# Optimization experiments

Hardware: AMD Instinct MI355X
Metric: run time of the kernel (lower is better)

Reference implementation:

```python
import jax, jax.numpy as jnp
import numpy as np

DIM = 192
HEADS = 8
B, H, W = 2, 256, 256
CPH = DIM // HEADS  # 24 channels per head
EPS = 1e-12

_SOB_DX = np.array([[1, 0, 1], [-2, 0, 2], [-1, 0, 1]], np.float32)
_SOB_DY = np.array([[1, -2, -1], [0, 0, 0], [1, 2, 1]], np.float32)


def _conv2d(x, w, pad, groups=1):
    return jax.lax.conv_general_dilated(
        x, w, window_strides=(1, 1), padding=[(pad, pad), (pad, pad)],
        dimension_numbers=('NCHW', 'OIHW', 'NCHW'), feature_group_count=groups)


def _l2norm(t):
    n = jnp.sqrt(jnp.sum(t * t, axis=-1, keepdims=True))
    return t / jnp.maximum(n, EPS)


def _topk_masked_softmax(attn, k):
    # attn: [B, HEADS, C, C]; keep top-k entries per row, softmax over them.
    b, h, c, _ = attn.shape
    idx = jax.lax.top_k(attn, k)[1]                      # [B,H,C,k]
    flat_idx = idx.reshape(-1, k)
    rows = jnp.arange(flat_idx.shape[0])[:, None]
    mask = jnp.zeros((b * h * c, c), bool).at[rows, flat_idx].set(True)
    masked = jnp.where(mask.reshape(attn.shape), attn, -jnp.inf)
    return jax.nn.softmax(masked, axis=-1)


def setup_inputs() -> dict:
    key = jax.random.key(0)
    ks = jax.random.split(key, 6)
    s = 0.02
    return {
        'x': jax.random.normal(ks[0], (B, DIM, H, W), jnp.float32),
        'q_w': jax.random.normal(ks[1], (DIM, DIM, 1, 1), jnp.float32) * s,
        'q_dw': jax.random.normal(ks[2], (DIM, 1, 3, 3), jnp.float32) * s,
        'kv_w': jax.random.normal(ks[3], (2 * DIM, DIM, 1, 1), jnp.float32) * s,
        'kv_dw': jax.random.normal(ks[4], (2 * DIM, 1, 3, 3), jnp.float32) * s,
        'proj_w': jax.random.normal(ks[5], (DIM, DIM, 1, 1), jnp.float32) * s,
        'temperature': jnp.ones((HEADS, 1, 1), jnp.float32),
        'a1': jnp.full((1,), 0.2, jnp.float32),
        'a2': jnp.full((1,), 0.2, jnp.float32),
        'a3': jnp.full((1,), 0.2, jnp.float32),
        'a4': jnp.full((1,), 0.2, jnp.float32),
    }


def reference(x, q_w, q_dw, kv_w, kv_dw, proj_w, temperature, a1, a2, a3, a4):
    b, c, h, w = x.shape
    # Sob: dense (dim,dim,3,3) Sobel convs (kernel broadcast over all in-channels)
    dx_w = jnp.broadcast_to(jnp.asarray(_SOB_DX), (c, c, 3, 3))
    dy_w = jnp.broadcast_to(jnp.asarray(_SOB_DY), (c, c, 3, 3))
    dx = _conv2d(x, dx_w, 1)
    dy = _conv2d(x, dy_w, 1)

    q_s = _conv2d(_conv2d(dx + dy, q_w, 0), q_dw, 1, groups=c)
    kv = _conv2d(_conv2d(x, kv_w, 0), kv_dw, 1, groups=2 * c)
    k_, v = kv[:, :c], kv[:, c:]

    hw = h * w
    q_s = _l2norm(q_s.reshape(b, HEADS, CPH, hw))
    k_ = _l2norm(k_.reshape(b, HEADS, CPH, hw))
    v = v.reshape(b, HEADS, CPH, hw)

    # channel attention: [B, HEADS, C, C]
    attn = jnp.einsum('bhcn,bhdn->bhcd', q_s, k_) * temperature

    C = CPH
    out = (a1 * (_topk_masked_softmax(attn, int(C / 2)) @ v)
           + a2 * (_topk_masked_softmax(attn, int(C * 2 / 3)) @ v)
           + a3 * (_topk_masked_softmax(attn, int(C * 3 / 4)) @ v)
           + a4 * (_topk_masked_softmax(attn, int(C * 4 / 5)) @ v))

    out = out.reshape(b, c, h, w)
    return _conv2d(out, proj_w, 0)
```

## Files before the change

kernel.cpp:

```cpp
#include <hip/hip_runtime.h>
#include <math.h>

#define NH 8
#define HWv 65536
#define C2 384

typedef __attribute__((ext_vector_type(8))) short bf16x8;
typedef __attribute__((ext_vector_type(4))) float f32x4;

__device__ __forceinline__ float bf2f(unsigned short u) {
    union { unsigned int i; float f; } v; v.i = ((unsigned int)u) << 16; return v.f;
}
__device__ __forceinline__ unsigned short f2bf(float f) {
    union { float f; unsigned int i; } v; v.f = f;
    unsigned int r = v.i + 0x7fff + ((v.i >> 16) & 1);
    return (unsigned short)(r >> 16);
}
__device__ __forceinline__ float hi_of(float a) {
    union { float f; unsigned int i; } u; u.f = a; u.i &= 0xffff0000u; return u.f;
}
__device__ __forceinline__ unsigned short hi16(float a) {
    union { float f; unsigned int i; } u; u.f = a; return (unsigned short)(u.i >> 16);
}
__device__ __forceinline__ unsigned int pack_hi2(float a, float b) {
    union { float f; unsigned int i; } ua, ub; ua.f = a; ub.f = b;
    return (ua.i >> 16) | (ub.i & 0xffff0000u);
}
__device__ __forceinline__ void gld16(const void* g, void* l) {
    __builtin_amdgcn_global_load_lds(
        (const __attribute__((address_space(1))) unsigned int*)g,
        (__attribute__((address_space(3))) unsigned int*)l, 16, 0, 0);
}
__device__ __forceinline__ int rot4(int lb, int row) {
    return (lb + row + (row >> 2)) & 3;
}

__global__ __launch_bounds__(256) void k_wprep(const float* __restrict__ w,
                                               const float* __restrict__ qw,
                                               unsigned short* __restrict__ oh,
                                               unsigned short* __restrict__ ol,
                                               float* __restrict__ qs) {
    if (blockIdx.x == 288) {
        const int o = threadIdx.x;
        if (o < 192) {
            float s = 0.f;
            for (int i = 0; i < 192; ++i) s += qw[(size_t)o * 192 + i];
            qs[o] = s;
        }
        return;
    }
    const int i = blockIdx.x * 256 + threadIdx.x;
    const int e = i & 7, jp = (i >> 3) & 3, rowidx = i >> 5;
    const int o = rowidx % 384, ks = rowidx / 384;
    const int lb = (jp - o - (o >> 2)) & 3;
    const int k = ks * 32 + (lb << 3) + e;
    const float v = w[(size_t)o * 192 + k];
    const unsigned short h = f2bf(v);
    oh[i] = h;
    ol[i] = f2bf(v - bf2f(h));
}

__global__ __launch_bounds__(256, 2) void k_gemm(const float* __restrict__ x,
                                                 const unsigned short* __restrict__ wh,
                                                 const unsigned short* __restrict__ wl,
                                                 unsigned short* __restrict__ t,
                                                 float* __restrict__ s) {
    const int l = blockIdx.x;
    const int xcd = l & 7, idx = l >> 3;
    const int pxtile = xcd * 64 + (idx >> 1);
    const int half = idx & 1;
    const int b = blockIdx.z;
    const int p0 = pxtile * 128;
    const int woff = half * 192;
    const int tid = threadIdx.x;
    const int lane = tid & 63, wv = tid >> 6;
    const int wm2 = wv & 1, wn2 = wv >> 1;
    __shared__ __align__(16) char SU[40960];
    unsigned short* Xh  = (unsigned short*)SU;
    unsigned short* Xl  = Xh + 128 * 32;
    unsigned short* Whs = Xl + 128 * 32;
    unsigned short* Wls = Whs + 192 * 32;
    unsigned short* Ts  = (unsigned short*)SU;
    float* Ls = (float*)(SU + 26624);
    f32x4 acc[4][6];
#pragma unroll
    for (int m = 0; m < 4; ++m)
#pragma unroll
        for (int n = 0; n < 6; ++n) acc[m][n] = (f32x4){0.f, 0.f, 0.f, 0.f};
    const int px = tid & 127, cg = tid >> 7;
    const float* xb = x + (size_t)b * 192 * HWv + p0 + px;
    const int r = lane & 15, g = lane >> 4;
    const int pbx0 = rot4(2 * cg, px);
    const int pbx1 = rot4(2 * cg + 1, px);
    float csum = 0.f;
    for (int ks = 0; ks < 6; ++ks) {
        const int k0 = ks * 32;
        __syncthreads();
        {
            const char* gh  = (const char*)wh + ((size_t)(ks * 384 + woff)) * 64;
            const char* gl2 = (const char*)wl + ((size_t)(ks * 384 + woff)) * 64;
            char* lh = (char*)Whs;
            char* ll = (char*)Wls;
#pragma unroll
            for (int i = 0; i < 3; ++i) {
                const int chunk = (i * 4 + wv) * 1024;
                gld16(gh + chunk + lane * 16, lh + chunk);
                gld16(gl2 + chunk + lane * 16, ll + chunk);
            }
        }
        {
            unsigned int ph[8], pl[8];
#pragma unroll
            for (int i2 = 0; i2 < 8; ++i2) {
                const int c0 = k0 + cg * 16 + i2 * 2;
                const float v0 = xb[(size_t)c0 * HWv];
                const float v1 = xb[(size_t)(c0 + 1) * HWv];
                csum += v0 + v1;
                ph[i2] = pack_hi2(v0, v1);
                pl[i2] = pack_hi2(v0 - hi_of(v0), v1 - hi_of(v1));
            }
            *(uint4*)&Xh[px * 32 + pbx0 * 8] = make_uint4(ph[0], ph[1], ph[2], ph[3]);
            *(uint4*)&Xh[px * 32 + pbx1 * 8] = make_uint4(ph[4], ph[5], ph[6], ph[7]);
            *(uint4*)&Xl[px * 32 + pbx0 * 8] = make_uint4(pl[0], pl[1], pl[2], pl[3]);
            *(uint4*)&Xl[px * 32 + pbx1 * 8] = make_uint4(pl[4], pl[5], pl[6], pl[7]);
        }
        __syncthreads();
        bf16x8 ah[4], al[4];
#pragma unroll
        for (int m = 0; m < 4; ++m) {
            const int row = wm2 * 64 + m * 16 + r;
            const int ro = rot4(g, row) * 8;
            ah[m] = *(const bf16x8*)&Xh[row * 32 + ro];
            al[m] = *(const bf16x8*)&Xl[row * 32 + ro];
        }
#pragma unroll
        for (int n = 0; n < 6; ++n) {
            const int row = wn2 * 96 + n * 16 + r;
            const int ro = rot4(g, row) * 8;
            const bf16x8 bh = *(const bf16x8*)&Whs[row * 32 + ro];
            const bf16x8 bl = *(const bf16x8*)&Wls[row * 32 + ro];
#pragma unroll
            for (int m = 0; m < 4; ++m) {
                acc[m][n] = __builtin_amdgcn_mfma_f32_16x16x32_bf16(ah[m], bh, acc[m][n], 0, 0, 0);
                acc[m][n] = __builtin_amdgcn_mfma_f32_16x16x32_bf16(ah[m], bl, acc[m][n], 0, 0, 0);
                acc[m][n] = __builtin_amdgcn_mfma_f32_16x16x32_bf16(al[m], bh, acc[m][n], 0, 0, 0);
            }
        }
    }
    __syncthreads();
    if (half == 0) Ls[cg * 128 + px] = csum;
    __syncthreads();
    if (half == 0 && tid < 128)
        s[((size_t)b << 16) + p0 + tid] = Ls[tid] + Ls[128 + tid];
    unsigned short* tb = t + (size_t)b * HWv * C2;
#pragma unroll
    for (int ph2 = 0; ph2 < 2; ++ph2) {
        __syncthreads();
        if (wm2 == ph2) {
#pragma unroll
            for (int m = 0; m < 4; ++m)
#pragma unroll
                for (int n = 0; n < 6; ++n)
#pragma unroll
                    for (int rr = 0; rr < 4; ++rr)
                        Ts[(m * 16 + g * 4 + rr) * 200 + wn2 * 96 + n * 16 + r] =
                            f2bf(acc[m][n][rr]);
        }
        __syncthreads();
        for (int i = tid; i < 1536; i += 256) {
            const int pxl = i / 24, cho = (i % 24) * 8;
            unsigned short* dst = tb + (size_t)(p0 + ph2 * 64 + pxl) * C2 + woff + cho;
            *(uint4*)dst = *(const uint4*)&Ts[pxl * 200 + cho];
        }
    }
}

__global__ __launch_bounds__(256) void k_attn(const unsigned short* __restrict__ t,
                                              const float* __restrict__ sbuf,
                                              const float* __restrict__ qsum,
                                              const float* __restrict__ qdw,
                                              const float* __restrict__ kvdw,
                                              float* __restrict__ part) {
    const int z = blockIdx.z, b = z >> 3, h = z & 7;
    const int tid = threadIdx.x;
    const int lane = tid & 63, wv = tid >> 6;
    __shared__ __align__(16) char U[50688];
    float* ehalo = (float*)U;
    float* Thalo = (float*)(U + 1296);
    float* shalo = (float*)(U + 32496);
    unsigned short* QKh = (unsigned short*)U;
    unsigned short* QKl = QKh + 48 * 264;
    float* Pp = (float*)U;
    __shared__ float qdwl[216], kdwl[216], qsml[24];
    for (int i = tid; i < 456; i += 256) {
        if (i < 216) qdwl[i] = qdw[h * 216 + i];
        else if (i < 432) kdwl[i - 216] = kvdw[h * 216 + (i - 216)];
        else qsml[i - 432] = qsum[h * 24 + (i - 432)];
    }
    f32x4 acc[6];
#pragma unroll
    for (int tl = 0; tl < 6; ++tl) acc[tl] = (f32x4){0.f, 0.f, 0.f, 0.f};
    const int lr = tid >> 4, lc = tid & 15;
    const int r = lane & 15, g = lane >> 4;
    for (int st = 0; st < 4; ++st) {
        const int tx0 = (blockIdx.x * 2 + (st & 1)) * 16;
        const int ty0 = (blockIdx.y * 2 + (st >> 1)) * 16;
        __syncthreads();
        for (int i = tid; i < 400; i += 256) {
            const int rr = i / 20, cc = i % 20;
            const int y = ty0 - 2 + rr, xx = tx0 - 2 + cc;
            shalo[i] = (y >= 0 && y < 256 && xx >= 0 && xx < 256)
                           ? sbuf[((size_t)b << 16) + y * 256 + xx] : 0.f;
        }
        for (int i = tid; i < 972; i += 256) {
            const int p = i / 3, seg = i % 3;
            const int rr = p / 18, cc = p % 18;
            const int y = ty0 - 1 + rr, xx = tx0 - 1 + cc;
            if (y >= 0 && y < 256 && xx >= 0 && xx < 256) {
                const unsigned short* src =
                    t + ((size_t)b * HWv + y * 256 + xx) * C2 + h * 24 + seg * 8;
                const uint4 v = *(const uint4*)src;
                Thalo[(seg * 8 + 0) * 325 + p] = bf2f((unsigned short)(v.x & 0xffff));
                Thalo[(seg * 8 + 1) * 325 + p] = bf2f((unsigned short)(v.x >> 16));
                Thalo[(seg * 8 + 2) * 325 + p] = bf2f((unsigned short)(v.y & 0xffff));
                Thalo[(seg * 8 + 3) * 325 + p] = bf2f((unsigned short)(v.y >> 16));
                Thalo[(seg * 8 + 4) * 325 + p] = bf2f((unsigned short)(v.z & 0xffff));
                Thalo[(seg * 8 + 5) * 325 + p] = bf2f((unsigned short)(v.z >> 16));
                Thalo[(seg * 8 + 6) * 325 + p] = bf2f((unsigned short)(v.w & 0xffff));
                Thalo[(seg * 8 + 7) * 325 + p] = bf2f((unsigned short)(v.w >> 16));
            } else {
#pragma unroll
                for (int j = 0; j < 8; ++j) Thalo[(seg * 8 + j) * 325 + p] = 0.f;
            }
        }
        __syncthreads();
        for (int i = tid; i < 324; i += 256) {
            const int rr = i / 18, cc = i % 18;
            const int y = ty0 - 1 + rr, xx = tx0 - 1 + cc;
            const float v = (((((shalo[rr * 20 + cc]
                              - shalo[rr * 20 + cc + 1])
                              - shalo[(rr + 1) * 20 + cc])
                              + shalo[(rr + 1) * 20 + cc + 2])
                              + shalo[(rr + 2) * 20 + cc + 1])
                              + shalo[(rr + 2) * 20 + cc + 2]);
            ehalo[i] = (y >= 0 && y < 256 && xx >= 0 && xx < 256) ? 2.f * v : 0.f;
        }
        __syncthreads();
        float qreg[24], kreg[24];
#pragma unroll
        for (int c = 0; c < 24; ++c) {
            float aq = 0.f, ak = 0.f;
#pragma unroll
            for (int dy = 0; dy < 3; ++dy)
#pragma unroll
                for (int dx = 0; dx < 3; ++dx) {
                    aq = fmaf(qdwl[c * 9 + dy * 3 + dx], ehalo[(lr + dy) * 18 + lc + dx], aq);
                    ak = fmaf(kdwl[c * 9 + dy * 3 + dx], Thalo[c * 325 + (lr + dy) * 18 + lc + dx], ak);
                }
            qreg[c] = qsml[c] * aq;
            kreg[c] = ak;
        }
        __syncthreads();
#pragma unroll
        for (int c = 0; c < 24; ++c) {
            const float q = qreg[c], kv = kreg[c];
            QKh[c * 264 + tid] = hi16(q);
            QKl[c * 264 + tid] = hi16(q - hi_of(q));
            QKh[(24 + c) * 264 + tid] = hi16(kv);
            QKl[(24 + c) * 264 + tid] = hi16(kv - hi_of(kv));
        }
        __syncthreads();
#pragma unroll
        for (int c2 = 0; c2 < 2; ++c2) {
            const int colb = (wv * 2 + c2) * 32 + g * 8;
            bf16x8 fh[3], fl[3];
#pragma unroll
            for (int rt = 0; rt < 3; ++rt) {
                fh[rt] = *(const bf16x8*)&QKh[(rt * 16 + r) * 264 + colb];
                fl[rt] = *(const bf16x8*)&QKl[(rt * 16 + r) * 264 + colb];
            }
#define GRAM(T, A, B) \
    acc[T] = __builtin_amdgcn_mfma_f32_16x16x32_bf16(fh[A], fh[B], acc[T], 0, 0, 0); \
    acc[T] = __builtin_amdgcn_mfma_f32_16x16x32_bf16(fh[A], fl[B], acc[T], 0, 0, 0); \
    acc[T] = __builtin_amdgcn_mfma_f32_16x16x32_bf16(fl[A], fh[B], acc[T], 0, 0, 0);
            GRAM(0, 0, 0) GRAM(1, 0, 1) GRAM(2, 0, 2)
            GRAM(3, 1, 1) GRAM(4, 1, 2) GRAM(5, 2, 2)
#undef GRAM
        }
    }
    __syncthreads();
#pragma unroll
    for (int tl = 0; tl < 6; ++tl)
#pragma unroll
        for (int reg = 0; reg < 4; ++reg)
            Pp[wv * 1536 + tl * 256 + (g * 4 + reg) * 16 + r] = acc[tl][reg];
    __syncthreads();
    float* dst = part + ((size_t)z * 64 + blockIdx.y * 8 + blockIdx.x) * 1536;
    for (int i = tid; i < 1536; i += 256)
        dst[i] = Pp[i] + Pp[1536 + i] + Pp[3072 + i] + Pp[4608 + i];
}

__device__ __forceinline__ int gidx(int i, int j) {
    const int rt = i >> 4, ct = j >> 4;
    const int tl = (rt == 0) ? ct : (rt == 1 ? 2 + ct : 5);
    return tl * 256 + (i & 15) * 16 + (j & 15);
}

__global__ __launch_bounds__(256) void k_redcomb(const float* __restrict__ part,
                                                 const float* __restrict__ temp,
                                                 const float* __restrict__ a1,
                                                 const float* __restrict__ a2,
                                                 const float* __restrict__ a3,
                                                 const float* __restrict__ a4,
                                                 float* __restrict__ Wg) {
    const int z = blockIdx.x, b = z >> 3, h = z & 7;
    const int tid = threadIdx.x;
    __shared__ float S[1536];
    __shared__ float att[24][24];
    __shared__ float nq[24], nk[24];
    for (int i = tid; i < 1536; i += 256) {
        float sum = 0.f;
        const float* p = part + (size_t)z * 64 * 1536 + i;
        for (int blk = 0; blk < 64; ++blk) sum += p[(size_t)blk * 1536];
        S[i] = sum;
    }
    __syncthreads();
    if (tid < 24) nq[tid] = fmaxf(sqrtf(S[gidx(tid, tid)]), 1e-12f);
    else if (tid >= 32 && tid < 56) {
        const int d = tid - 32;
        nk[d] = fmaxf(sqrtf(S[gidx(24 + d, 24 + d)]), 1e-12f);
    }
    __syncthreads();
    const float tp = temp[h];
    for (int op = tid; op < 576; op += 256) {
        const int c = op / 24, d = op % 24;
        att[c][d] = S[gidx(c, 24 + d)] * tp / (nq[c] * nk[d]);
    }
    __syncthreads();
    if (tid < 24) {
        const int c = tid;
        float v[24];
#pragma unroll
        for (int d = 0; d < 24; ++d) v[d] = att[c][d];
        int rank[24];
#pragma unroll
        for (int d = 0; d < 24; ++d) {
            int rr = 0;
#pragma unroll
            for (int d2 = 0; d2 < 24; ++d2)
                rr += (v[d2] > v[d]) || (v[d2] == v[d] && d2 < d);
            rank[d] = rr;
        }
        const int ks[4] = {12, 16, 18, 19};
        const float as[4] = {a1[0], a2[0], a3[0], a4[0]};
        float w[24] = {};
        for (int ti = 0; ti < 4; ++ti) {
            const int kk = ks[ti];
            float m = -1e30f;
            for (int d = 0; d < 24; ++d) if (rank[d] < kk) m = fmaxf(m, v[d]);
            float Z = 0.f, ex[24];
            for (int d = 0; d < 24; ++d) {
                ex[d] = (rank[d] < kk) ? expf(v[d] - m) : 0.f;
                Z += ex[d];
            }
            const float sc = as[ti] / Z;
            for (int d = 0; d < 24; ++d) w[d] += ex[d] * sc;
        }
        for (int d = 0; d < 24; ++d)
            Wg[(((size_t)b * NH + h) * 24 + c) * 24 + d] = w[d];
    }
}

__global__ void k_makeM(const float* __restrict__ projw, const float* __restrict__ Wg,
                        unsigned short* __restrict__ Mh, unsigned short* __restrict__ Ml) {
    const int b = blockIdx.x / 192, o = blockIdx.x % 192;
    const int j = threadIdx.x;
    const int h = j / 24, d = j % 24;
    float s = 0.f;
#pragma unroll
    for (int cc = 0; cc < 24; ++cc)
        s = fmaf(projw[(size_t)o * 192 + h * 24 + cc],
                 Wg[(((size_t)b * NH + h) * 24 + cc) * 24 + d], s);
    const unsigned short hh = f2bf(s);
    const int jg = j >> 5, jb = (j >> 3) & 3, e = j & 7;
    const int jp = rot4(jb, o);
    const size_t dst = (((size_t)b * 6 + jg) * 192 + o) * 32 + jp * 8 + e;
    Mh[dst] = hh;
    Ml[dst] = f2bf(s - bf2f(hh));
}

__global__ __launch_bounds__(256) void k_final(const unsigned short* __restrict__ t,
                                               const float* __restrict__ kvdw,
                                               const unsigned short* __restrict__ Mh,
                                               const unsigned short* __restrict__ Ml,
                                               float* __restrict__ out) {
    const int b = blockIdx.y;
    const int tile = blockIdx.x;
    const int x0 = (tile & 15) * 16, y0 = (tile >> 4) * 4;
    const int tid = threadIdx.x;
    const int lane = tid & 63, wv = tid >> 6;
    __shared__ __align__(16) unsigned short Th[108][40];
    __shared__ __align__(16) unsigned short Msh[192 * 32], Msl[192 * 32];
    __shared__ __align__(16) unsigned short Vsh[64][40], Vsl[64][40];
    __shared__ float Wdl[288];
    f32x4 acc[3][4];
#pragma unroll
    for (int m = 0; m < 3; ++m)
#pragma unroll
        for (int n = 0; n < 4; ++n) acc[m][n] = (f32x4){0.f, 0.f, 0.f, 0.f};
    const int px = tid & 63, jq = tid >> 6;
    const int lx = px & 15, ly = px >> 4;
    const int r = lane & 15, g = lane >> 4;
    for (int jg = 0; jg < 6; ++jg) {
        const int j0 = jg * 32;
        __syncthreads();
        {
            const char* gh  = (const char*)Mh + (((size_t)b * 6 + jg) * 192) * 64;
            const char* gl2 = (const char*)Ml + (((size_t)b * 6 + jg) * 192) * 64;
            char* lh = (char*)Msh;
            char* ll = (char*)Msl;
#pragma unroll
            for (int i = 0; i < 3; ++i) {
                const int chunk = (i * 4 + wv) * 1024;
                gld16(gh + chunk + lane * 16, lh + chunk);
                gld16(gl2 + chunk + lane * 16, ll + chunk);
            }
        }
        if (tid < 216) {
            const int hp = tid >> 1, half = tid & 1;
            const int hy = hp / 18, hx = hp % 18;
            const int y = y0 - 1 + hy, xx = x0 - 1 + hx;
            uint4 v0 = make_uint4(0, 0, 0, 0), v1 = make_uint4(0, 0, 0, 0);
            if (y >= 0 && y < 256 && xx >= 0 && xx < 256) {
                const unsigned short* src =
                    t + ((size_t)b * HWv + y * 256 + xx) * C2 + 192 + j0 + half * 16;
                v0 = *(const uint4*)src;
                v1 = *(const uint4*)(src + 8);
            }
            *(uint4*)&Th[hp][half * 16] = v0;
            *(uint4*)&Th[hp][half * 16 + 8] = v1;
        }
        for (int i = tid; i < 288; i += 256) Wdl[i] = kvdw[1728 + jg * 288 + i];
        __syncthreads();
        {
            float vv[8] = {0.f, 0.f, 0.f, 0.f, 0.f, 0.f, 0.f, 0.f};
#pragma unroll
            for (int dy = 0; dy < 3; ++dy)
#pragma unroll
                for (int dx = 0; dx < 3; ++dx) {
                    const int hp = (ly + dy) * 18 + lx + dx;
                    const uint4 tv = *(const uint4*)&Th[hp][jq * 8];
                    float tf[8];
                    tf[0] = bf2f((unsigned short)(tv.x & 0xffff));
                    tf[1] = bf2f((unsigned short)(tv.x >> 16));
                    tf[2] = bf2f((unsigned short)(tv.y & 0xffff));
                    tf[3] = bf2f((unsigned short)(tv.y >> 16));
                    tf[4] = bf2f((unsigned short)(tv.z & 0xffff));
                    tf[5] = bf2f((unsigned short)(tv.z >> 16));
                    tf[6] = bf2f((unsigned short)(tv.w & 0xffff));
                    tf[7] = bf2f((unsigned short)(tv.w >> 16));
                    const int tap = dy * 3 + dx;
#pragma unroll
                    for (int jj = 0; jj < 8; ++jj)
                        vv[jj] = fmaf(Wdl[(jq * 8 + jj) * 9 + tap], tf[jj], vv[jj]);
                }
            unsigned int ph[4], pl[4];
#pragma unroll
            for (int i2 = 0; i2 < 4; ++i2) {
                const float a = vv[i2 * 2], c = vv[i2 * 2 + 1];
                ph[i2] = pack_hi2(a, c);
                pl[i2] = pack_hi2(a - hi_of(a), c - hi_of(c));
            }
            *(uint4*)&Vsh[px][jq * 8] = make_uint4(ph[0], ph[1], ph[2], ph[3]);
            *(uint4*)&Vsl[px][jq * 8] = make_uint4(pl[0], pl[1], pl[2], pl[3]);
        }
        __syncthreads();
        bf16x8 bh[4], bl[4];
#pragma unroll
        for (int n = 0; n < 4; ++n) {
            bh[n] = *(const bf16x8*)&Vsh[n * 16 + r][g * 8];
            bl[n] = *(const bf16x8*)&Vsl[n * 16 + r][g * 8];
        }
#pragma unroll
        for (int m = 0; m < 3; ++m) {
            const int row = wv * 48 + m * 16 + r;
            const int ro = rot4(g, row) * 8;
            const bf16x8 ah = *(const bf16x8*)&Msh[row * 32 + ro];
            const bf16x8 al = *(const bf16x8*)&Msl[row * 32 + ro];
#pragma unroll
            for (int n = 0; n < 4; ++n) {
                acc[m][n] = __builtin_amdgcn_mfma_f32_16x16x32_bf16(ah, bh[n], acc[m][n], 0, 0, 0);
                acc[m][n] = __builtin_amdgcn_mfma_f32_16x16x32_bf16(ah, bl[n], acc[m][n], 0, 0, 0);
                acc[m][n] = __builtin_amdgcn_mfma_f32_16x16x32_bf16(al, bh[n], acc[m][n], 0, 0, 0);
            }
        }
    }
#pragma unroll
    for (int m = 0; m < 3; ++m) {
        const int o = wv * 48 + m * 16 + g * 4;
#pragma unroll
        for (int n = 0; n < 4; ++n) {
            const int p = (y0 + n) * 256 + x0 + r;
#pragma unroll
            for (int rr = 0; rr < 4; ++rr)
                out[((size_t)b * 192 + o + rr) * HWv + p] = acc[m][n][rr];
        }
    }
}


extern "C" void kernel_launch(void* const* d_in, const int* in_sizes, int n_in,
                              void* d_out, int out_size, void* d_ws, size_t ws_size,
                              hipStream_t stream) {
    (void)in_sizes; (void)n_in; (void)out_size;
    const float* x     = (const float*)d_in[0];
    const float* qw    = (const float*)d_in[1];
    const float* qdw   = (const float*)d_in[2];
    const float* kvw   = (const float*)d_in[3];
    const float* kvdw  = (const float*)d_in[4];
    const float* projw = (const float*)d_in[5];
    const float* temp  = (const float*)d_in[6];
    const float* a1    = (const float*)d_in[7];
    const float* a2    = (const float*)d_in[8];
    const float* a3    = (const float*)d_in[9];
    const float* a4    = (const float*)d_in[10];
    float* out = (float*)d_out;

    const size_t T_EL = (size_t)2 * HWv * C2;
    const size_t needB = T_EL * 2
                       + (size_t)(131072 + 131072 + 192 + 1572864 + 24576 + 9216) * 4
                       + (size_t)(73728 * 4) * 2;
    if (ws_size < needB) return;
    unsigned short* t = (unsigned short*)d_ws;
    float* s    = (float*)(t + T_EL);
    float* e    = s + 131072;
    float* qsum = e + 131072;
    float* part = qsum + 192;
    float* accS = part + 1572864;
    float* Wg   = accS + 24576;
    unsigned short* wh = (unsigned short*)(Wg + 9216);
    unsigned short* wl = wh + 73728;
    unsigned short* Mh = wl + 73728;
    unsigned short* Ml = Mh + 73728;

    k_wprep<<<289, 256, 0, stream>>>(kvw, qw, wh, wl, qsum);
    k_gemm<<<dim3(1024, 1, 2), 256, 0, stream>>>(x, wh, wl, t, s);
    k_attn<<<dim3(8, 8, 16), 256, 0, stream>>>(t, s, qsum, qdw, kvdw, part);
    k_redcomb<<<16, 256, 0, stream>>>(part, temp, a1, a2, a3, a4, Wg);
    k_makeM<<<384, 192, 0, stream>>>(projw, Wg, Mh, Ml);
    k_final<<<dim3(1024, 2), 256, 0, stream>>>(t, kvdw, Mh, Ml, out);
}
```

Baseline: 256.1 us.

## Double-buffer weight tiles in LDS and prefetch x into registers in GEMM

The 1x1-conv GEMM kernel now keeps two LDS buffers for the hi/lo bf16 weight tiles and a two-slot register buffer for x. Each k-step issues the loads for step k+1 before converting and computing step k, so global latency overlaps with MFMA work instead of sitting behind a __syncthreads. The paired __syncthreads are replaced by raw s_barrier calls plus an explicit lgkmcnt wait. This raises LDS use from 40 KB to 64 KB per block and adds register pressure from the 32-float prefetch buffer, and it relies on compiler-inserted vmcnt waits to make the async LDS loads visible before they are read.

New measurement: 267.0 us. 4.3% more time.

```diff
diff --git a/kernel.cpp b/kernel.cpp
--- a/kernel.cpp
+++ b/kernel.cpp
@@ -75,11 +75,9 @@
     const int tid = threadIdx.x;
     const int lane = tid & 63, wv = tid >> 6;
     const int wm2 = wv & 1, wn2 = wv >> 1;
-    __shared__ __align__(16) char SU[40960];
+    __shared__ __align__(16) char SU[65536];
     unsigned short* Xh  = (unsigned short*)SU;
-    unsigned short* Xl  = Xh + 128 * 32;
-    unsigned short* Whs = Xl + 128 * 32;
-    unsigned short* Wls = Whs + 192 * 32;
+    unsigned short* Xl  = (unsigned short*)(SU + 8192);
     unsigned short* Ts  = (unsigned short*)SU;
     float* Ls = (float*)(SU + 26624);
     f32x4 acc[4][6];
@@ -93,28 +91,54 @@
     const int pbx0 = rot4(2 * cg, px);
     const int pbx1 = rot4(2 * cg + 1, px);
     float csum = 0.f;
+    float xr[2][16];
+
+    {
+        const char* gh  = (const char*)wh + ((size_t)woff) * 64;
+        const char* gl2 = (const char*)wl + ((size_t)woff) * 64;
+        char* wbase = SU + 16384;
+#pragma unroll
+        for (int i = 0; i < 3; ++i) {
+            const int chunk = (i * 4 + wv) * 1024;
+            gld16(gh + chunk + lane * 16, wbase + chunk);
+            gld16(gl2 + chunk + lane * 16, wbase + 12288 + chunk);
+        }
+#pragma unroll
+        for (int i2 = 0; i2 < 8; ++i2) {
+            const int c0 = cg * 16 + i2 * 2;
+            xr[0][2 * i2]     = xb[(size_t)c0 * HWv];
+            xr[0][2 * i2 + 1] = xb[(size_t)(c0 + 1) * HWv];
+        }
+    }
+
+#pragma unroll
     for (int ks = 0; ks < 6; ++ks) {
-        const int k0 = ks * 32;
-        __syncthreads();
-        {
-            const char* gh  = (const char*)wh + ((size_t)(ks * 384 + woff)) * 64;
-            const char* gl2 = (const char*)wl + ((size_t)(ks * 384 + woff)) * 64;
-            char* lh = (char*)Whs;
-            char* ll = (char*)Wls;
+        const int cur = ks & 1, nxt = cur ^ 1;
+        asm volatile("" ::: "memory");
+        __builtin_amdgcn_s_barrier();
+        asm volatile("" ::: "memory");
+        if (ks < 5) {
+            const char* gh  = (const char*)wh + ((size_t)((ks + 1) * 384 + woff)) * 64;
+            const char* gl2 = (const char*)wl + ((size_t)((ks + 1) * 384 + woff)) * 64;
+            char* wbase = SU + 16384 + nxt * 24576;
 #pragma unroll
             for (int i = 0; i < 3; ++i) {
                 const int chunk = (i * 4 + wv) * 1024;
-                gld16(gh + chunk + lane * 16, lh + chunk);
-                gld16(gl2 + chunk + lane * 16, ll + chunk);
+                gld16(gh + chunk + lane * 16, wbase + chunk);
+                gld16(gl2 + chunk + lane * 16, wbase + 12288 + chunk);
+            }
+#pragma unroll
+            for (int i2 = 0; i2 < 8; ++i2) {
+                const int c0 = (ks + 1) * 32 + cg * 16 + i2 * 2;
+                xr[nxt][2 * i2]     = xb[(size_t)c0 * HWv];
+                xr[nxt][2 * i2 + 1] = xb[(size_t)(c0 + 1) * HWv];
             }
         }
         {
             unsigned int ph[8], pl[8];
 #pragma unroll
             for (int i2 = 0; i2 < 8; ++i2) {
-                const int c0 = k0 + cg * 16 + i2 * 2;
-                const float v0 = xb[(size_t)c0 * HWv];
-                const float v1 = xb[(size_t)(c0 + 1) * HWv];
+                const float v0 = xr[cur][2 * i2], v1 = xr[cur][2 * i2 + 1];
                 csum += v0 + v1;
                 ph[i2] = pack_hi2(v0, v1);
                 pl[i2] = pack_hi2(v0 - hi_of(v0), v1 - hi_of(v1));
@@ -124,7 +148,12 @@
             *(uint4*)&Xl[px * 32 + pbx0 * 8] = make_uint4(pl[0], pl[1], pl[2], pl[3]);
             *(uint4*)&Xl[px * 32 + pbx1 * 8] = make_uint4(pl[4], pl[5], pl[6], pl[7]);
         }
-        __syncthreads();
+        asm volatile("s_waitcnt lgkmcnt(0)" ::: "memory");
+        __builtin_amdgcn_s_barrier();
+        asm volatile("" ::: "memory");
+        const unsigned short* Whs =
+            (const unsigned short*)(SU + 16384 + cur * 24576);
+        const unsigned short* Wls = Whs + 6144;
         bf16x8 ah[4], al[4];
 #pragma unroll
         for (int m = 0; m < 4; ++m) {
```
